# Performance work log

Measured on AMD Instinct MI355X. Metric: run time of the kernel, lower is better.

Reference implementation:

```python
import jax, jax.numpy as jnp
import numpy as np

N_INST, BATCH, IN_DIM, L_DIM = 256, 128, 1024, 512

def setup_inputs() -> dict:
    key = jax.random.key(0)
    k1, k2, k3, k4 = jax.random.split(key, 4)
    # glorot-uniform-ish scales
    sv = np.sqrt(6.0 / (IN_DIM + L_DIM)).astype(np.float32)
    sw = np.sqrt(6.0 / (L_DIM + 1)).astype(np.float32)
    x = jax.random.normal(k1, (N_INST, BATCH, IN_DIM), dtype=jnp.float32)
    v = jax.random.uniform(k2, (IN_DIM, L_DIM), minval=-sv, maxval=sv, dtype=jnp.float32)
    u = jax.random.uniform(k3, (IN_DIM, L_DIM), minval=-sv, maxval=sv, dtype=jnp.float32)
    w = jax.random.uniform(k4, (L_DIM, 1), minval=-sw, maxval=sw, dtype=jnp.float32)
    return {"x": x, "v": v, "u": u, "w": w}

def reference(x, v, u, w):
    # x: [n_instances, batch, in_dim]
    # Fused batched version of the per-instance loop:
    # score_i = (tanh(x_i @ v) * sigmoid(x_i @ u)) @ w, softmax over instances.
    h = jnp.tanh(jnp.einsum('nbd,dl->nbl', x, v))          # [n, b, l]
    g = jax.nn.sigmoid(jnp.einsum('nbd,dl->nbl', x, u))    # [n, b, l]
    scores = jnp.einsum('nbl,lo->nbo', h * g, w)            # [n, b, 1]
    alpha = jax.nn.softmax(scores, axis=0)                  # softmax over instance axis
    return alpha
```

## Files before the change

### kernel.cpp

```cpp
#include <hip/hip_runtime.h>
#include <stdint.h>

typedef unsigned int  u32;
typedef unsigned short u16;
typedef __bf16 v8bf __attribute__((ext_vector_type(8)));
typedef float  v4f  __attribute__((ext_vector_type(4)));

#define N_INST 256
#define BATCH  128
#define IN_DIM 1024
#define L_DIM  512
#define M_TOT  (N_INST*BATCH)

#define BM 128
#define BN 128
#define BK 64
#define KITERS (IN_DIM/BK)
#define NSLICE 16

#define XB_BYTES   ((size_t)M_TOT * IN_DIM * 2)
#define WPK_BYTES  ((size_t)1024 * IN_DIM * 2)

__device__ inline u32 f2bf_pk(float a, float b){
  u32 ua = __builtin_bit_cast(u32, a);
  u32 ub = __builtin_bit_cast(u32, b);
  ua = (ua + 0x7FFFu + ((ua >> 16) & 1u)) >> 16;
  ub = (ub + 0x7FFFu + ((ub >> 16) & 1u)) & 0xFFFF0000u;
  return ua | ub;
}

__device__ inline void gl2lds16(const u16* g, u16* l){
  __builtin_amdgcn_global_load_lds(
      (const __attribute__((address_space(1))) u32*)(g),
      (__attribute__((address_space(3))) u32*)(l), 16, 0, 0);
}

#define PREP_XBLKS 16384
__global__ void prep(const float* __restrict__ x, const float* __restrict__ v,
                     const float* __restrict__ u, u16* __restrict__ xb,
                     u16* __restrict__ wpk){
  const int b = blockIdx.x;
  if (b < PREP_XBLKS){
    size_t o = ((size_t)b * 256 + threadIdx.x) * 8;
    float4 a0 = *reinterpret_cast<const float4*>(x + o);
    float4 a1 = *reinterpret_cast<const float4*>(x + o + 4);
    uint4 out;
    out.x = f2bf_pk(a0.x, a0.y); out.y = f2bf_pk(a0.z, a0.w);
    out.z = f2bf_pk(a1.x, a1.y); out.w = f2bf_pk(a1.z, a1.w);
    *reinterpret_cast<uint4*>(xb + o) = out;
  } else {
    int t = (b - PREP_XBLKS) * 256 + threadIdx.x;
    int o = t * 8;
    int np = o >> 10;
    int k0 = o & 1023;
    int l  = ((np >> 5) << 4) | (np & 15);
    const float* src = ((np >> 4) & 1) ? u : v;
    u32 out[4];
#pragma unroll
    for (int i = 0; i < 4; ++i){
      float a = src[(size_t)(k0 + 2*i    ) * L_DIM + l];
      float c = src[(size_t)(k0 + 2*i + 1) * L_DIM + l];
      out[i] = f2bf_pk(a, c);
    }
    *reinterpret_cast<uint4*>(wpk + o) = make_uint4(out[0], out[1], out[2], out[3]);
  }
}

__launch_bounds__(256)
__global__ void gemm_score(const u16* __restrict__ xb, const u16* __restrict__ wpk,
                           const float* __restrict__ w, float* __restrict__ partial){
  __shared__ __align__(16) u16 As[BM * BK];
  __shared__ __align__(16) u16 Bs[BN * BK];

  const int tid  = threadIdx.x;
  const int nblk = blockIdx.x;
  const int mblk = blockIdx.y;
  const int m0   = mblk * BM;

  const int lane = tid & 63;
  const int wave = tid >> 6;
  const int wm   = (wave >> 1) * 64;
  const int wn   = (wave & 1) * 64;
  const int q    = lane >> 4;
  const int c    = lane & 15;

  const int rr = lane >> 3;
  const int cg = (lane & 7) ^ rr;
  const u16* ga = xb  + (size_t)m0 * IN_DIM;
  const u16* gb = wpk + (size_t)(nblk * BN) * IN_DIM;

  int aoff[4], boff[4];
#pragma unroll
  for (int i = 0; i < 4; ++i){
    const int ra = wm + i*16 + c;
    aoff[i] = ra*64 + ((q ^ (ra & 7)) * 8);
    const int rb = wn + i*16 + c;
    boff[i] = rb*64 + ((q ^ (rb & 7)) * 8);
  }

  v4f acc[4][4];
#pragma unroll
  for (int i = 0; i < 4; ++i)
#pragma unroll
    for (int j = 0; j < 4; ++j)
      acc[i][j] = (v4f){0.f, 0.f, 0.f, 0.f};

  for (int kt = 0; kt < KITERS; ++kt){
    const int kb = kt * BK;
#pragma unroll
    for (int j = 0; j < 4; ++j){
      const int reg = wave * 4 + j;
      const int row = reg * 8 + rr;
      gl2lds16(ga + (size_t)row * IN_DIM + kb + cg * 8, &As[reg * 512 + lane * 8]);
      gl2lds16(gb + (size_t)row * IN_DIM + kb + cg * 8, &Bs[reg * 512 + lane * 8]);
    }
    __syncthreads();
#pragma unroll
    for (int kk = 0; kk < 2; ++kk){
      v8bf af[4], bfr[4];
#pragma unroll
      for (int i = 0; i < 4; ++i){
        af[i]  = *reinterpret_cast<const v8bf*>(&As[aoff[i] ^ (kk*32)]);
        bfr[i] = *reinterpret_cast<const v8bf*>(&Bs[boff[i] ^ (kk*32)]);
      }
#pragma unroll
      for (int i = 0; i < 4; ++i)
#pragma unroll
        for (int j = 0; j < 4; ++j)
          acc[i][j] = __builtin_amdgcn_mfma_f32_16x16x32_bf16(af[i], bfr[j], acc[i][j], 0, 0, 0);
    }
    __syncthreads();
  }

  const int lbase = nblk*64 + (wn >> 5)*16 + c;
  const float wl0 = w[lbase];
  const float wl1 = w[lbase + 16];
  const int p = nblk*2 + (wn >> 6);
  float* pout = partial + (size_t)p * M_TOT + m0 + wm;

#pragma unroll
  for (int i = 0; i < 4; ++i){
#pragma unroll
    for (int r = 0; r < 4; ++r){
      float t0 = 2.f / (1.f + __expf(-2.f * acc[i][0][r])) - 1.f;
      float s0 = 1.f / (1.f + __expf(-acc[i][1][r]));
      float t1 = 2.f / (1.f + __expf(-2.f * acc[i][2][r])) - 1.f;
      float s1 = 1.f / (1.f + __expf(-acc[i][3][r]));
      float v2 = t0*s0*wl0 + t1*s1*wl1;
      v2 += __shfl_xor(v2, 1, 64);
      v2 += __shfl_xor(v2, 2, 64);
      v2 += __shfl_xor(v2, 4, 64);
      v2 += __shfl_xor(v2, 8, 64);
      if (c == 0) pout[i*16 + q*4 + r] = v2;
    }
  }
}

__global__ void softmax_inst(const float* __restrict__ partial, float* __restrict__ out){
  __shared__ float red[N_INST];
  const int b = blockIdx.x;
  const int n = threadIdx.x;
  float s = 0.f;
#pragma unroll
  for (int i = 0; i < NSLICE; ++i) s += partial[(size_t)i * M_TOT + n*BATCH + b];
  red[n] = s; __syncthreads();
  for (int st = N_INST/2; st > 0; st >>= 1){
    if (n < st) red[n] = fmaxf(red[n], red[n + st]);
    __syncthreads();
  }
  float mx = red[0]; __syncthreads();
  float e = __expf(s - mx);
  red[n] = e; __syncthreads();
  for (int st = N_INST/2; st > 0; st >>= 1){
    if (n < st) red[n] += red[n + st];
    __syncthreads();
  }
  out[n*BATCH + b] = e / red[0];
}

extern "C" void kernel_launch(void* const* d_in, const int* in_sizes, int n_in,
                              void* d_out, int out_size, void* d_ws, size_t ws_size,
                              hipStream_t stream) {
  const float* x = (const float*)d_in[0];
  const float* v = (const float*)d_in[1];
  const float* u = (const float*)d_in[2];
  const float* w = (const float*)d_in[3];
  u16*   xb      = (u16*)d_ws;
  u16*   wpk     = (u16*)((char*)d_ws + XB_BYTES);
  float* partial = (float*)((char*)d_ws + XB_BYTES + WPK_BYTES);
  float* out     = (float*)d_out;

  prep<<<dim3(PREP_XBLKS + 512), dim3(256), 0, stream>>>(x, v, u, xb, wpk);
  gemm_score<<<dim3(8, 256), dim3(256), 0, stream>>>(xb, wpk, w, partial);
  softmax_inst<<<dim3(BATCH), dim3(N_INST), 0, stream>>>(partial, out);
}
```

Before: 314.5 us.

## Pre-pack operands into MFMA fragment order and load directly from global to registers

The prep kernel now writes x and the packed v/u weights in the exact per-lane MFMA fragment layout, so the GEMM loads each fragment with one coalesced 16-byte global load per lane. Shared memory staging and both barriers per k-iteration are gone. Blocks are also remapped to a 1D grid so that consecutive blocks on each XCD share the same M-tile and reuse it in L2. The cost is no sharing of A/B tiles between waves through LDS: each wave re-reads its operands from L2/global, and the k-loop has no explicit prefetch, which risks exposed memory latency.

```diff
diff --git a/kernel.cpp b/kernel.cpp
--- a/kernel.cpp
+++ b/kernel.cpp
@@ -29,74 +29,65 @@
   return ua | ub;
 }
 
-__device__ inline void gl2lds16(const u16* g, u16* l){
-  __builtin_amdgcn_global_load_lds(
-      (const __attribute__((address_space(1))) u32*)(g),
-      (__attribute__((address_space(3))) u32*)(l), 16, 0, 0);
-}
-
 #define PREP_XBLKS 16384
 __global__ void prep(const float* __restrict__ x, const float* __restrict__ v,
                      const float* __restrict__ u, u16* __restrict__ xb,
                      u16* __restrict__ wpk){
   const int b = blockIdx.x;
   if (b < PREP_XBLKS){
-    size_t o = ((size_t)b * 256 + threadIdx.x) * 8;
-    float4 a0 = *reinterpret_cast<const float4*>(x + o);
-    float4 a1 = *reinterpret_cast<const float4*>(x + o + 4);
+    int t = b * 256 + threadIdx.x;
+    int r = t >> 6, l = t & 63;
+    int kk = r & 1, i = (r >> 1) & 3, h = (r >> 3) & 1, kt = (r >> 4) & 15, mb = r >> 8;
+    int q = l >> 4, c = l & 15;
+    int row = mb*128 + h*64 + i*16 + c;
+    int k0  = kt*64 + kk*32 + q*8;
+    const float* src = x + (size_t)row * IN_DIM + k0;
+    float4 a0 = *reinterpret_cast<const float4*>(src);
+    float4 a1 = *reinterpret_cast<const float4*>(src + 4);
     uint4 out;
     out.x = f2bf_pk(a0.x, a0.y); out.y = f2bf_pk(a0.z, a0.w);
     out.z = f2bf_pk(a1.x, a1.y); out.w = f2bf_pk(a1.z, a1.w);
-    *reinterpret_cast<uint4*>(xb + o) = out;
+    *reinterpret_cast<uint4*>(xb + (size_t)r*512 + l*8) = out;
   } else {
     int t = (b - PREP_XBLKS) * 256 + threadIdx.x;
-    int o = t * 8;
-    int np = o >> 10;
-    int k0 = o & 1023;
-    int l  = ((np >> 5) << 4) | (np & 15);
-    const float* src = ((np >> 4) & 1) ? u : v;
-    u32 out[4];
+    int r = t >> 6, l = t & 63;
+    int kk = r & 1, j = (r >> 1) & 3, h = (r >> 3) & 1, kt = (r >> 4) & 15, nb = r >> 8;
+    int q = l >> 4, c = l & 15;
+    int bcol = nb*8 + h*4 + j;
+    const float* src = (bcol & 1) ? u : v;
+    int lcol = (bcol >> 1)*16 + c;
+    int k0 = kt*64 + kk*32 + q*8;
+    u32 o[4];
 #pragma unroll
-    for (int i = 0; i < 4; ++i){
-      float a = src[(size_t)(k0 + 2*i    ) * L_DIM + l];
-      float c = src[(size_t)(k0 + 2*i + 1) * L_DIM + l];
-      out[i] = f2bf_pk(a, c);
+    for (int ii = 0; ii < 4; ++ii){
+      float a  = src[(size_t)(k0 + 2*ii    ) * L_DIM + lcol];
+      float bb = src[(size_t)(k0 + 2*ii + 1) * L_DIM + lcol];
+      o[ii] = f2bf_pk(a, bb);
     }
-    *reinterpret_cast<uint4*>(wpk + o) = make_uint4(out[0], out[1], out[2], out[3]);
+    *reinterpret_cast<uint4*>(wpk + (size_t)r*512 + l*8) = make_uint4(o[0], o[1], o[2], o[3]);
   }
 }
 
 __launch_bounds__(256)
 __global__ void gemm_score(const u16* __restrict__ xb, const u16* __restrict__ wpk,
                            const float* __restrict__ w, float* __restrict__ partial){
-  __shared__ __align__(16) u16 As[BM * BK];
-  __shared__ __align__(16) u16 Bs[BN * BK];
-
   const int tid  = threadIdx.x;
-  const int nblk = blockIdx.x;
-  const int mblk = blockIdx.y;
+  const u32 bid  = blockIdx.x;
+  const int xcd  = bid & 7;
+  const int slot = bid >> 3;
+  const int nblk = slot & 7;
+  const int mblk = xcd * 32 + (slot >> 3);
   const int m0   = mblk * BM;
 
   const int lane = tid & 63;
   const int wave = tid >> 6;
-  const int wm   = (wave >> 1) * 64;
-  const int wn   = (wave & 1) * 64;
+  const int ha   = wave >> 1;
+  const int hb   = wave & 1;
   const int q    = lane >> 4;
   const int c    = lane & 15;
 
-  const int rr = lane >> 3;
-  const int cg = (lane & 7) ^ rr;
-  const u16* ga = xb  + (size_t)m0 * IN_DIM;
-  const u16* gb = wpk + (size_t)(nblk * BN) * IN_DIM;
-
-  int aoff[4], boff[4];
-#pragma unroll
-  for (int i = 0; i < 4; ++i){
-    const int ra = wm + i*16 + c;
-    aoff[i] = ra*64 + ((q ^ (ra & 7)) * 8);
-    const int rb = wn + i*16 + c;
-    boff[i] = rb*64 + ((q ^ (rb & 7)) * 8);
-  }
+  const u16* pa = xb  + (size_t)mblk*131072 + ha*4096 + lane*8;
+  const u16* pb = wpk + (size_t)nblk*131072 + hb*4096 + lane*8;
 
   v4f acc[4][4];
 #pragma unroll
@@ -105,38 +96,30 @@
     for (int j = 0; j < 4; ++j)
       acc[i][j] = (v4f){0.f, 0.f, 0.f, 0.f};
 
+#pragma unroll 1
   for (int kt = 0; kt < KITERS; ++kt){
-    const int kb = kt * BK;
+    const u16* a = pa + kt*8192;
+    const u16* b = pb + kt*8192;
+    v8bf af[8], bfr[8];
 #pragma unroll
-    for (int j = 0; j < 4; ++j){
-      const int reg = wave * 4 + j;
-      const int row = reg * 8 + rr;
-      gl2lds16(ga + (size_t)row * IN_DIM + kb + cg * 8, &As[reg * 512 + lane * 8]);
-      gl2lds16(gb + (size_t)row * IN_DIM + kb + cg * 8, &Bs[reg * 512 + lane * 8]);
+    for (int f = 0; f < 8; ++f){
+      af[f]  = *reinterpret_cast<const v8bf*>(a + f*512);
+      bfr[f] = *reinterpret_cast<const v8bf*>(b + f*512);
     }
-    __syncthreads();
 #pragma unroll
-    for (int kk = 0; kk < 2; ++kk){
-      v8bf af[4], bfr[4];
-#pragma unroll
-      for (int i = 0; i < 4; ++i){
-        af[i]  = *reinterpret_cast<const v8bf*>(&As[aoff[i] ^ (kk*32)]);
-        bfr[i] = *reinterpret_cast<const v8bf*>(&Bs[boff[i] ^ (kk*32)]);
-      }
+    for (int kk = 0; kk < 2; ++kk)
 #pragma unroll
       for (int i = 0; i < 4; ++i)
 #pragma unroll
         for (int j = 0; j < 4; ++j)
-          acc[i][j] = __builtin_amdgcn_mfma_f32_16x16x32_bf16(af[i], bfr[j], acc[i][j], 0, 0, 0);
-    }
-    __syncthreads();
+          acc[i][j] = __builtin_amdgcn_mfma_f32_16x16x32_bf16(af[i*2+kk], bfr[j*2+kk], acc[i][j], 0, 0, 0);
   }
 
-  const int lbase = nblk*64 + (wn >> 5)*16 + c;
+  const int lbase = nblk*64 + hb*32 + c;
   const float wl0 = w[lbase];
   const float wl1 = w[lbase + 16];
-  const int p = nblk*2 + (wn >> 6);
-  float* pout = partial + (size_t)p * M_TOT + m0 + wm;
+  const int p = nblk*2 + hb;
+  float* pout = partial + (size_t)p * M_TOT + m0 + ha*64;
 
 #pragma unroll
   for (int i = 0; i < 4; ++i){
@@ -191,6 +174,6 @@
   float* out     = (float*)d_out;
 
   prep<<<dim3(PREP_XBLKS + 512), dim3(256), 0, stream>>>(x, v, u, xb, wpk);
-  gemm_score<<<dim3(8, 256), dim3(256), 0, stream>>>(xb, wpk, w, partial);
+  gemm_score<<<dim3(2048), dim3(256), 0, stream>>>(xb, wpk, w, partial);
   softmax_inst<<<dim3(BATCH), dim3(N_INST), 0, stream>>>(partial, out);
 }
```

New measurement: 303.4 us. 3.5% less time.
